# Kernel tuning notes

Measured on AMD Instinct MI355X. Metric: run time of the kernel, lower is better.

## Reference

```python
import jax, jax.numpy as jnp
from jax import lax
import numpy as np

B, T, D, H, OUT = 64, 1024, 256, 512, 256

def _uniform(key, shape, bound):
    return jax.random.uniform(key, shape, jnp.float32, -bound, bound)

def setup_inputs() -> dict:
    key = jax.random.key(0)
    ks = jax.random.split(key, 12)
    bnd = 1.0 / np.sqrt(H)
    inp = {
        "input": jax.random.normal(ks[0], (B, T, D), jnp.float32),
        # layer 0: input_size -> hidden_size
        "W_ih0": _uniform(ks[1], (4 * H, D), bnd),
        "W_hh0": _uniform(ks[2], (4 * H, H), bnd),
        "b_ih0": _uniform(ks[3], (4 * H,), bnd),
        "b_hh0": _uniform(ks[4], (4 * H,), bnd),
        # layer 1: hidden_size -> hidden_size
        "W_ih1": _uniform(ks[5], (4 * H, H), bnd),
        "W_hh1": _uniform(ks[6], (4 * H, H), bnd),
        "b_ih1": _uniform(ks[7], (4 * H,), bnd),
        "b_hh1": _uniform(ks[8], (4 * H,), bnd),
        # final projection
        "fc_w": _uniform(ks[9], (OUT, H), bnd),
        "fc_b": _uniform(ks[10], (OUT,), bnd),
    }
    return inp

def _lstm_layer(x_seq, W_ih, W_hh, b_ih, b_hh):
    # x_seq: [T, B, Din] -> hidden sequence [T, B, H]
    Bb = x_seq.shape[1]
    Hh = W_hh.shape[1]
    # precompute input-to-hidden projection for all timesteps (one big GEMM)
    xW = jnp.einsum("tbd,gd->tbg", x_seq, W_ih) + b_ih + b_hh  # [T, B, 4H]

    def step(carry, xw):
        h, c = carry
        gates = xw + h @ W_hh.T  # [B, 4H]
        i, f, g, o = jnp.split(gates, 4, axis=-1)
        c_new = jax.nn.sigmoid(f) * c + jax.nn.sigmoid(i) * jnp.tanh(g)
        h_new = jax.nn.sigmoid(o) * jnp.tanh(c_new)
        return (h_new, c_new), h_new

    init = (jnp.zeros((Bb, Hh), x_seq.dtype), jnp.zeros((Bb, Hh), x_seq.dtype))
    _, hs = lax.scan(step, init, xW)
    return hs  # [T, B, H]

def reference(input, W_ih0, W_hh0, b_ih0, b_hh0, W_ih1, W_hh1, b_ih1, b_hh1, fc_w, fc_b):
    x = jnp.transpose(input, (1, 0, 2))  # [T, B, D], matches input.permute(1,0,2)
    h1 = _lstm_layer(x, W_ih0, W_hh0, b_ih0, b_hh0)   # layer 0 over all timesteps
    h2 = _lstm_layer(h1, W_ih1, W_hh1, b_ih1, b_hh1)  # layer 1 consumes layer-0 outputs
    last = h2[-1]  # outs[-1].squeeze(): [B, H] (squeeze is a no-op here)
    return last @ fc_w.T + fc_b  # [B, OUT]
```

## Files before the change

### kernel.cpp

```cpp
#include <hip/hip_runtime.h>
#include <hip/hip_bf16.h>
#include <stdint.h>

typedef short short8 __attribute__((ext_vector_type(8)));
typedef float f32x4  __attribute__((ext_vector_type(4)));
typedef float fvec4  __attribute__((ext_vector_type(4)));

#define SCOPE_AGENT __HIP_MEMORY_SCOPE_AGENT
#define MFMA(a,b,c) __builtin_amdgcn_mfma_f32_16x16x32_bf16((a),(b),(c),0,0,0)

constexpr int nT = 1024, nD = 256, nH = 512, nO = 256;
constexpr int SLOT_ELEMS = 64 * 1024;
constexpr size_t SLOT_BYTES = (size_t)SLOT_ELEMS * 2;
constexpr size_t RING_OFF = 8192;
constexpr int NEG = -0x40000000;

#define K4(M)  M(0) M(1) M(2) M(3)
#define GK2(M) M(0,0) M(1,0) M(2,0) M(3,0) M(0,1) M(1,1) M(2,1) M(3,1)
#define GK4(M) GK2(M) M(0,2) M(1,2) M(2,2) M(3,2) M(0,3) M(1,3) M(2,3) M(3,3)

__device__ __forceinline__ float sigm(float x){ return 1.f/(1.f + __expf(-x)); }

__device__ __forceinline__ short8 cvt8h(const float* p){
  fvec4 a = *(const fvec4*)p;
  fvec4 b = *(const fvec4*)(p + 4);
  short8 hi;
  #pragma unroll
  for (int j = 0; j < 8; j++){
    float v = (j < 4) ? a[j] : b[j-4];
    hi[j] = (short)__bfloat16_as_ushort(__float2bfloat16(v));
  }
  return hi;
}

__device__ __forceinline__ void cvt8(const float* p, short8& hi, short8& lo){
  fvec4 a = *(const fvec4*)p;
  fvec4 b = *(const fvec4*)(p + 4);
  #pragma unroll
  for (int j = 0; j < 8; j++){
    float v = (j < 4) ? a[j] : b[j-4];
    __hip_bfloat16 h = __float2bfloat16(v);
    float r = v - __bfloat162float(h);
    hi[j] = (short)__bfloat16_as_ushort(h);
    lo[j] = (short)__bfloat16_as_ushort(__float2bfloat16(r));
  }
}

__device__ __forceinline__ unsigned pack2(float a, float b){
  return (unsigned)__bfloat16_as_ushort(__float2bfloat16(a)) |
         ((unsigned)__bfloat16_as_ushort(__float2bfloat16(b)) << 16);
}
__device__ __forceinline__ unsigned pack2lo(float a, float b){
  float ra = a - __bfloat162float(__float2bfloat16(a));
  float rb = b - __bfloat162float(__float2bfloat16(b));
  return pack2(ra, rb);
}

template<int FAST>
__device__ __forceinline__ short8 ldh(const short* p){
  if constexpr (FAST){
    return *(const short8*)p;
  } else {
    union { unsigned long long u[2]; short8 v; } r;
    const unsigned long long* q = (const unsigned long long*)p;
    r.u[0] = __hip_atomic_load(q,     __ATOMIC_RELAXED, SCOPE_AGENT);
    r.u[1] = __hip_atomic_load(q + 1, __ATOMIC_RELAXED, SCOPE_AGENT);
    return r.v;
  }
}

__device__ __forceinline__ void poll(const int* fb, int t0, int t1){
  if (threadIdx.x < 64){
    int lid = threadIdx.x;
    int tgt = (lid < 32) ? t0 : t1;
    const int* p = fb + lid;
    int spins = 0;
    for(;;){
      int v = __hip_atomic_load(p, __ATOMIC_RELAXED, SCOPE_AGENT);
      if (__all(v >= tgt)) break;
      if (++spins > (1<<17)) break;
      if (spins > 64) __builtin_amdgcn_s_sleep(1);
    }
  }
  __syncthreads();
}

template<int FAST>
__global__ __launch_bounds__(256, 1)
__attribute__((amdgpu_waves_per_eu(1, 1)))
void lstm_kernel(
    const float* __restrict__ x,
    const float* __restrict__ Wih0, const float* __restrict__ Whh0,
    const float* __restrict__ bih0, const float* __restrict__ bhh0,
    const float* __restrict__ Wih1, const float* __restrict__ Whh1,
    const float* __restrict__ bih1, const float* __restrict__ bhh1,
    const float* __restrict__ fcw, const float* __restrict__ fcb,
    float* __restrict__ out,
    short* __restrict__ h1r, short* __restrict__ h2r,
    float* __restrict__ h2last, int* __restrict__ flags, int* __restrict__ arrive)
{
  constexpr int S1M = FAST ? 31 : 7;
  constexpr int S2M = FAST ? 31 : 3;
  constexpr int BPS = FAST ? 24 : 8;

  const int bid   = blockIdx.x;
  const int layer = bid & 1;
  const int bs    = (bid >> 1) & 3;
  const int ns    = bid >> 3;
  const int tid   = threadIdx.x;
  const int w     = tid >> 6;
  const int l     = tid & 63;
  const int lm    = l & 15;
  const int ke    = (l >> 4) << 3;
  const int kw4   = w << 2;
  const int kw2   = w << 1;

  int* fb     = flags + (bs << 6);
  int* myflag = fb + (layer << 5) + ns;

  __shared__ float glds[4][4][16][17];

  __builtin_amdgcn_fence(__ATOMIC_SEQ_CST, "agent");
  __syncthreads();
  if (tid == 0) __hip_atomic_fetch_add(arrive, 1, __ATOMIC_RELAXED, SCOPE_AGENT);
  if (tid < 64){
    int spins = 0;
    while (__hip_atomic_load(arrive, __ATOMIC_RELAXED, SCOPE_AGENT) < 256){
      if (++spins > (1<<20)) break;
      __builtin_amdgcn_s_sleep(1);
    }
  }
  __syncthreads();

  #define GCOL(g) ((g<<9) + (ns<<4) + lm)
  const int brow = (bs << 4) + lm;
  const int bl   = tid >> 4, jj = tid & 15;
  const int hcolbase = ns << 4;

  float c_reg = 0.f;
  float bia0, bia1, bia2, bia3;
  {
    const float* bi = layer ? bih1 : bih0;
    const float* bh = layer ? bhh1 : bhh0;
    int c0 = (ns<<4) + jj;
    bia0 = bi[c0]      + bh[c0];
    bia1 = bi[512+c0]  + bh[512+c0];
    bia2 = bi[1024+c0] + bh[1024+c0];
    bia3 = bi[1536+c0] + bh[1536+c0];
  }

  #define GWR(g) { _Pragma("unroll")                                            \
    for (int r = 0; r < 4; r++) glds[w][g][((l>>4)<<2)+r][lm] = p##g[r]; }
  #define CELLX(SLOTBASE, T, LAST)                                              \
  {                                                                             \
    GWR(0) GWR(1) GWR(2) GWR(3)                                                 \
    __syncthreads();                                                            \
    float gi = glds[0][0][bl][jj]+glds[1][0][bl][jj]+glds[2][0][bl][jj]+glds[3][0][bl][jj]+bia0; \
    float gf = glds[0][1][bl][jj]+glds[1][1][bl][jj]+glds[2][1][bl][jj]+glds[3][1][bl][jj]+bia1; \
    float gg = glds[0][2][bl][jj]+glds[1][2][bl][jj]+glds[2][2][bl][jj]+glds[3][2][bl][jj]+bia2; \
    float go = glds[0][3][bl][jj]+glds[1][3][bl][jj]+glds[2][3][bl][jj]+glds[3][3][bl][jj]+bia3; \
    float cn = sigm(gf)*c_reg + sigm(gi)*tanhf(gg);                             \
    c_reg = cn;                                                                 \
    float hn  = sigm(go)*tanhf(cn);                                             \
    float hn2 = __shfl_down(hn, 1);                                             \
    if (!(jj & 1)){                                                             \
      short* p = (SLOTBASE) + bl*1024 + hcolbase + jj;                          \
      __hip_atomic_store((unsigned*)p,       pack2(hn,hn2),   __ATOMIC_RELAXED, SCOPE_AGENT); \
      __hip_atomic_store((unsigned*)(p+512), pack2lo(hn,hn2), __ATOMIC_RELAXED, SCOPE_AGENT); \
    }                                                                           \
    if (LAST)                                                                   \
      __hip_atomic_store(h2last + (size_t)((bs<<4)+bl)*nH + hcolbase + jj, hn,  \
                         __ATOMIC_RELAXED, SCOPE_AGENT);                        \
    __syncthreads();             \
    if (tid == 0)                                                               \
      __hip_atomic_store(myflag, (T), __ATOMIC_RELAXED, SCOPE_AGENT);           \
  }

  if (layer == 0){
    #define DWX(g,i) short8 wxh##g##_##i;
    GK2(DWX)
    #define LWX(g,i) wxh##g##_##i = cvt8h(Wih0 + (size_t)GCOL(g)*nD + (kw2+i)*32 + ke);
    GK2(LWX)
    #define DWH(g,i) short8 whh##g##_##i;
    GK4(DWH)
    #define LWH(g,i) whh##g##_##i = cvt8h(Whh0 + (size_t)GCOL(g)*nH + (kw4+i)*32 + ke);
    GK4(LWH)

    f32x4 xc0={0,0,0,0}, xc1={0,0,0,0}, xc2={0,0,0,0}, xc3={0,0,0,0};
    {
      const float* xb = x + ((size_t)brow*nT)*nD + ke + kw2*32;
      short8 th0, tl0, th1, tl1;
      cvt8(xb, th0, tl0); cvt8(xb + 32, th1, tl1);
      #define XM0(g,i) xc##g = MFMA(th##i, wxh##g##_##i, xc##g);                \
                       xc##g = MFMA(tl##i, wxh##g##_##i, xc##g);
      GK2(XM0)
    }

    for (int t = 0; t < nT; t++){
      poll(fb, t-1, t-BPS);
      if constexpr (FAST)
        if ((t & 15) == 0) __builtin_amdgcn_fence(__ATOMIC_ACQUIRE, "agent");
      const short* hb = h1r + (size_t)((t+S1M)&S1M)*SLOT_ELEMS + brow*1024;
      #define HLD0(i) short8 vh##i = ldh<FAST>(hb + (kw4+i)*32 + ke);           \
                      short8 vl##i = ldh<FAST>(hb + 512 + (kw4+i)*32 + ke);
      K4(HLD0)
      f32x4 xn0={0,0,0,0}, xn1={0,0,0,0}, xn2={0,0,0,0}, xn3={0,0,0,0};
      if (t + 1 < nT){
        const float* xb = x + ((size_t)brow*nT + (t+1))*nD + ke + kw2*32;
        short8 th0, tl0, th1, tl1;
        cvt8(xb, th0, tl0); cvt8(xb + 32, th1, tl1);
        #define XMN(g,i) xn##g = MFMA(th##i, wxh##g##_##i, xn##g);              \
                         xn##g = MFMA(tl##i, wxh##g##_##i, xn##g);
        GK2(XMN)
      }
      f32x4 p0a=xc0, p1a=xc1, p2a=xc2, p3a=xc3;
      f32x4 p0b={0,0,0,0}, p1b={0,0,0,0}, p2b={0,0,0,0}, p3b={0,0,0,0};
      #define HMM0(g,i) { f32x4& d = (i<2) ? p##g##a : p##g##b;                 \
        d = MFMA(vh##i, whh##g##_##i, d); d = MFMA(vl##i, whh##g##_##i, d); }
      GK4(HMM0)
      f32x4 p0=p0a+p0b, p1=p1a+p1b, p2=p2a+p2b, p3=p3a+p3b;
      CELLX(h1r + (size_t)(t&S1M)*SLOT_ELEMS + (bs<<4)*1024, t, 0)
      xc0 = xn0; xc1 = xn1; xc2 = xn2; xc3 = xn3;
    }
  } else {
    #define DWA(g,i) short8 ahh##g##_##i;
    GK4(DWA)
    #define LWA(g,i) ahh##g##_##i = cvt8h(Whh1 + (size_t)GCOL(g)*nH + (kw4+i)*32 + ke);
    GK4(LWA)
    #define DWB(g,i) short8 bwh##g##_##i;
    GK4(DWB)
    #define LWB(g,i) bwh##g##_##i = cvt8h(Wih1 + (size_t)GCOL(g)*nH + (kw4+i)*32 + ke);
    GK4(LWB)

    for (int t = 0; t < nT; t++){
      poll(fb, t, t-1);
      if constexpr (FAST)
        if ((t & 15) == 0) __builtin_amdgcn_fence(__ATOMIC_ACQUIRE, "agent");
      const short* h2b = h2r + (size_t)((t+S2M)&S2M)*SLOT_ELEMS + brow*1024;
      const short* h1b = h1r + (size_t)(t&S1M)*SLOT_ELEMS + brow*1024;
      #define HLD2(i) short8 u2h##i = ldh<FAST>(h2b + (kw4+i)*32 + ke);         \
                      short8 u2l##i = ldh<FAST>(h2b + 512 + (kw4+i)*32 + ke);
      K4(HLD2)
      #define HLD1(i) short8 u1h##i = ldh<FAST>(h1b + (kw4+i)*32 + ke);         \
                      short8 u1l##i = ldh<FAST>(h1b + 512 + (kw4+i)*32 + ke);
      K4(HLD1)
      f32x4 p0a={0,0,0,0}, p1a={0,0,0,0}, p2a={0,0,0,0}, p3a={0,0,0,0};
      f32x4 p0b={0,0,0,0}, p1b={0,0,0,0}, p2b={0,0,0,0}, p3b={0,0,0,0};
      #define HMM2(g,i) { f32x4& d = (i<2) ? p##g##a : p##g##b;                 \
        d = MFMA(u2h##i, ahh##g##_##i, d); d = MFMA(u2l##i, ahh##g##_##i, d); }
      GK4(HMM2)
      #define HMM1(g,i) { f32x4& d = (i<2) ? p##g##a : p##g##b;                 \
        d = MFMA(u1h##i, bwh##g##_##i, d); d = MFMA(u1l##i, bwh##g##_##i, d); }
      GK4(HMM1)
      f32x4 p0=p0a+p0b, p1=p1a+p1b, p2=p2a+p2b, p3=p3a+p3b;
      CELLX(h2r + (size_t)(t&S2M)*SLOT_ELEMS + (bs<<4)*1024, t, (t == nT-1))
    }

    if (ns < 16){
      poll(fb, NEG, nT-1);
      const int orow = (bs<<4) + bl;
      const int ocol = (ns<<4) + jj;
      const unsigned long long* hq = (const unsigned long long*)(h2last + (size_t)orow*nH);
      const float* wr = fcw + (size_t)ocol*nH;
      float s0=0.f, s1=0.f, s2=0.f, s3=0.f;
      #pragma unroll 8
      for (int k = 0; k < nH; k += 8){
        union{ unsigned long long u; float f[2]; } q0,q1,q2,q3;
        q0.u = __hip_atomic_load(hq + (k>>1)    , __ATOMIC_RELAXED, SCOPE_AGENT);
        q1.u = __hip_atomic_load(hq + (k>>1) + 1, __ATOMIC_RELAXED, SCOPE_AGENT);
        q2.u = __hip_atomic_load(hq + (k>>1) + 2, __ATOMIC_RELAXED, SCOPE_AGENT);
        q3.u = __hip_atomic_load(hq + (k>>1) + 3, __ATOMIC_RELAXED, SCOPE_AGENT);
        fvec4 w0 = *(const fvec4*)(wr + k);
        fvec4 w1 = *(const fvec4*)(wr + k + 4);
        s0 += q0.f[0]*w0[0] + q0.f[1]*w0[1];
        s1 += q1.f[0]*w0[2] + q1.f[1]*w0[3];
        s2 += q2.f[0]*w1[0] + q2.f[1]*w1[1];
        s3 += q3.f[0]*w1[2] + q3.f[1]*w1[3];
      }
      out[(size_t)orow*nO + ocol] = s0 + s1 + s2 + s3 + fcb[ocol];
    }
  }
}

extern "C" void kernel_launch(void* const* d_in, const int* in_sizes, int n_in,
                              void* d_out, int out_size, void* d_ws, size_t ws_size,
                              hipStream_t stream)
{
  char* ws = (char*)d_ws;
  int* flags  = (int*)ws;
  int* arrive = (int*)(ws + 2048);

  size_t need_fast = RING_OFF + 64ull*SLOT_BYTES + (size_t)64*512*4 + 4096;
  const int fast = (ws_size >= need_fast) ? 1 : 0;
  const int s1 = fast ? 32 : 8, s2 = fast ? 32 : 4;

  short* h1r = (short*)(ws + RING_OFF);
  short* h2r = h1r + (size_t)s1 * SLOT_ELEMS;
  float* h2last = (float*)(h2r + (size_t)s2 * SLOT_ELEMS);

  hipMemsetAsync(ws, 0xFF, 1024, stream);
  hipMemsetAsync(ws + 2048, 0, 64, stream);
  hipMemsetAsync(h1r + (size_t)(s1-1)*SLOT_ELEMS, 0, SLOT_BYTES, stream);
  hipMemsetAsync(h2r + (size_t)(s2-1)*SLOT_ELEMS, 0, SLOT_BYTES, stream);

  const float* x    = (const float*)d_in[0];
  const float* Wih0 = (const float*)d_in[1];
  const float* Whh0 = (const float*)d_in[2];
  const float* bih0 = (const float*)d_in[3];
  const float* bhh0 = (const float*)d_in[4];
  const float* Wih1 = (const float*)d_in[5];
  const float* Whh1 = (const float*)d_in[6];
  const float* bih1 = (const float*)d_in[7];
  const float* bhh1 = (const float*)d_in[8];
  const float* fcw  = (const float*)d_in[9];
  const float* fcb  = (const float*)d_in[10];
  float* out = (float*)d_out;

  if (fast)
    lstm_kernel<1><<<256, 256, 0, stream>>>(x, Wih0, Whh0, bih0, bhh0,
        Wih1, Whh1, bih1, bhh1, fcw, fcb, out, h1r, h2r, h2last, flags, arrive);
  else
    lstm_kernel<0><<<256, 256, 0, stream>>>(x, Wih0, Whh0, bih0, bhh0,
        Wih1, Whh1, bih1, bhh1, fcw, fcb, out, h1r, h2r, h2last, flags, arrive);
}
```

Before: 4.546 ms.

## Use per-wave flags, split layer-1 polling, and widen hidden-state stores

Each wave now publishes its own progress flag after waiting on its own stores (vmcnt(0)), which removes the block-wide barrier before signalling. Layer 1 first waits only for layer-0 h1, runs that half of the MFMAs, and only then polls for its own previous h2 step. This overlaps the layer-0 dependency wait with compute. Hidden-state writes are packed into 64-bit atomic stores from every fourth lane. The flag array grows fourfold and pollers now read 128 flags per group, which adds polling traffic. The slow-path BPS also changes from 8 to 7.

```diff
diff --git a/kernel.cpp b/kernel.cpp
--- a/kernel.cpp
+++ b/kernel.cpp
@@ -13,7 +13,6 @@
 constexpr int SLOT_ELEMS = 64 * 1024;
 constexpr size_t SLOT_BYTES = (size_t)SLOT_ELEMS * 2;
 constexpr size_t RING_OFF = 8192;
-constexpr int NEG = -0x40000000;
 
 #define K4(M)  M(0) M(1) M(2) M(3)
 #define GK2(M) M(0,0) M(1,0) M(2,0) M(3,0) M(0,1) M(1,1) M(2,1) M(3,1)
@@ -32,7 +31,6 @@
   }
   return hi;
 }
-
 __device__ __forceinline__ void cvt8(const float* p, short8& hi, short8& lo){
   fvec4 a = *(const fvec4*)p;
   fvec4 b = *(const fvec4*)(p + 4);
@@ -45,7 +43,6 @@
     lo[j] = (short)__bfloat16_as_ushort(__float2bfloat16(r));
   }
 }
-
 __device__ __forceinline__ unsigned pack2(float a, float b){
   return (unsigned)__bfloat16_as_ushort(__float2bfloat16(a)) |
          ((unsigned)__bfloat16_as_ushort(__float2bfloat16(b)) << 16);
@@ -69,15 +66,35 @@
   }
 }
 
-__device__ __forceinline__ void poll(const int* fb, int t0, int t1){
+__device__ __forceinline__ void poll128(const int* b, int tgt){
   if (threadIdx.x < 64){
-    int lid = threadIdx.x;
-    int tgt = (lid < 32) ? t0 : t1;
-    const int* p = fb + lid;
+    const int* p0 = b + threadIdx.x;
+    const int* p1 = b + 64 + threadIdx.x;
     int spins = 0;
     for(;;){
-      int v = __hip_atomic_load(p, __ATOMIC_RELAXED, SCOPE_AGENT);
-      if (__all(v >= tgt)) break;
+      int a = __hip_atomic_load(p0, __ATOMIC_RELAXED, SCOPE_AGENT);
+      int c = __hip_atomic_load(p1, __ATOMIC_RELAXED, SCOPE_AGENT);
+      if (__all((a >= tgt) && (c >= tgt))) break;
+      if (++spins > (1<<17)) break;
+      if (spins > 64) __builtin_amdgcn_s_sleep(1);
+    }
+  }
+  __syncthreads();
+}
+__device__ __forceinline__ void poll_l0(const int* peers, int tp,
+                                        const int* bp, int tb){
+  if (threadIdx.x < 64){
+    const int* p0 = peers + threadIdx.x;
+    const int* p1 = peers + 64 + threadIdx.x;
+    const int* q0 = bp + threadIdx.x;
+    const int* q1 = bp + 64 + threadIdx.x;
+    int spins = 0;
+    for(;;){
+      int a = __hip_atomic_load(p0, __ATOMIC_RELAXED, SCOPE_AGENT);
+      int c = __hip_atomic_load(p1, __ATOMIC_RELAXED, SCOPE_AGENT);
+      int d = __hip_atomic_load(q0, __ATOMIC_RELAXED, SCOPE_AGENT);
+      int e = __hip_atomic_load(q1, __ATOMIC_RELAXED, SCOPE_AGENT);
+      if (__all((a >= tp) && (c >= tp) && (d >= tb) && (e >= tb))) break;
       if (++spins > (1<<17)) break;
       if (spins > 64) __builtin_amdgcn_s_sleep(1);
     }
@@ -101,7 +118,7 @@
 {
   constexpr int S1M = FAST ? 31 : 7;
   constexpr int S2M = FAST ? 31 : 3;
-  constexpr int BPS = FAST ? 24 : 8;
+  constexpr int BPS = FAST ? 24 : 7;
 
   const int bid   = blockIdx.x;
   const int layer = bid & 1;
@@ -115,8 +132,9 @@
   const int kw4   = w << 2;
   const int kw2   = w << 1;
 
-  int* fb     = flags + (bs << 6);
-  int* myflag = fb + (layer << 5) + ns;
+  int* fl0   = flags + (bs << 8);
+  int* fl1   = fl0 + 128;
+  int* myflag = flags + (bs << 8) + (layer << 7) + (ns << 2) + w;
 
   __shared__ float glds[4][4][16][17];
 
@@ -151,8 +169,7 @@
 
   #define GWR(g) { _Pragma("unroll")                                            \
     for (int r = 0; r < 4; r++) glds[w][g][((l>>4)<<2)+r][lm] = p##g[r]; }
-  #define CELLX(SLOTBASE, T, LAST)                                              \
-  {                                                                             \
+  #define CELL_GATES()                                                          \
     GWR(0) GWR(1) GWR(2) GWR(3)                                                 \
     __syncthreads();                                                            \
     float gi = glds[0][0][bl][jj]+glds[1][0][bl][jj]+glds[2][0][bl][jj]+glds[3][0][bl][jj]+bia0; \
@@ -161,19 +178,25 @@
     float go = glds[0][3][bl][jj]+glds[1][3][bl][jj]+glds[2][3][bl][jj]+glds[3][3][bl][jj]+bia3; \
     float cn = sigm(gf)*c_reg + sigm(gi)*tanhf(gg);                             \
     c_reg = cn;                                                                 \
-    float hn  = sigm(go)*tanhf(cn);                                             \
-    float hn2 = __shfl_down(hn, 1);                                             \
-    if (!(jj & 1)){                                                             \
+    float hn = sigm(go)*tanhf(cn);
+
+  #define STORE_H(SLOTBASE, T, LASTST)                                          \
+  {                                                                             \
+    float hn1 = __shfl_down(hn, 1);                                             \
+    unsigned u0  = pack2(hn, hn1),  ul0 = pack2lo(hn, hn1);                     \
+    unsigned u1  = __shfl_down(u0, 2), ul1 = __shfl_down(ul0, 2);               \
+    if (!(jj & 3)){                                                             \
       short* p = (SLOTBASE) + bl*1024 + hcolbase + jj;                          \
-      __hip_atomic_store((unsigned*)p,       pack2(hn,hn2),   __ATOMIC_RELAXED, SCOPE_AGENT); \
-      __hip_atomic_store((unsigned*)(p+512), pack2lo(hn,hn2), __ATOMIC_RELAXED, SCOPE_AGENT); \
+      __hip_atomic_store((unsigned long long*)p,                                \
+          (unsigned long long)u0 | ((unsigned long long)u1 << 32),              \
+          __ATOMIC_RELAXED, SCOPE_AGENT);                                       \
+      __hip_atomic_store((unsigned long long*)(p + 512),                        \
+          (unsigned long long)ul0 | ((unsigned long long)ul1 << 32),            \
+          __ATOMIC_RELAXED, SCOPE_AGENT);                                       \
     }                                                                           \
-    if (LAST)                                                                   \
-      __hip_atomic_store(h2last + (size_t)((bs<<4)+bl)*nH + hcolbase + jj, hn,  \
-                         __ATOMIC_RELAXED, SCOPE_AGENT);                        \
-    __syncthreads();             \
-    if (tid == 0)                                                               \
-      __hip_atomic_store(myflag, (T), __ATOMIC_RELAXED, SCOPE_AGENT);           \
+    LASTST                                                                      \
+    asm volatile("s_waitcnt vmcnt(0)" ::: "memory");         \
+    if (l == 0) __hip_atomic_store(myflag, (T), __ATOMIC_RELAXED, SCOPE_AGENT); \
   }
 
   if (layer == 0){
@@ -197,7 +220,7 @@
     }
 
     for (int t = 0; t < nT; t++){
-      poll(fb, t-1, t-BPS);
+      poll_l0(fl0, t-1, fl1, t-BPS);
       if constexpr (FAST)
         if ((t & 15) == 0) __builtin_amdgcn_fence(__ATOMIC_ACQUIRE, "agent");
       const short* hb = h1r + (size_t)((t+S1M)&S1M)*SLOT_ELEMS + brow*1024;
@@ -219,7 +242,8 @@
         d = MFMA(vh##i, whh##g##_##i, d); d = MFMA(vl##i, whh##g##_##i, d); }
       GK4(HMM0)
       f32x4 p0=p0a+p0b, p1=p1a+p1b, p2=p2a+p2b, p3=p3a+p3b;
-      CELLX(h1r + (size_t)(t&S1M)*SLOT_ELEMS + (bs<<4)*1024, t, 0)
+      CELL_GATES()
+      STORE_H(h1r + (size_t)(t&S1M)*SLOT_ELEMS + (bs<<4)*1024, t, )
       xc0 = xn0; xc1 = xn1; xc2 = xn2; xc3 = xn3;
     }
   } else {
@@ -233,31 +257,36 @@
     GK4(LWB)
 
     for (int t = 0; t < nT; t++){
-      poll(fb, t, t-1);
+      poll128(fl0, t);
       if constexpr (FAST)
         if ((t & 15) == 0) __builtin_amdgcn_fence(__ATOMIC_ACQUIRE, "agent");
-      const short* h2b = h2r + (size_t)((t+S2M)&S2M)*SLOT_ELEMS + brow*1024;
       const short* h1b = h1r + (size_t)(t&S1M)*SLOT_ELEMS + brow*1024;
-      #define HLD2(i) short8 u2h##i = ldh<FAST>(h2b + (kw4+i)*32 + ke);         \
-                      short8 u2l##i = ldh<FAST>(h2b + 512 + (kw4+i)*32 + ke);
-      K4(HLD2)
       #define HLD1(i) short8 u1h##i = ldh<FAST>(h1b + (kw4+i)*32 + ke);         \
                       short8 u1l##i = ldh<FAST>(h1b + 512 + (kw4+i)*32 + ke);
       K4(HLD1)
       f32x4 p0a={0,0,0,0}, p1a={0,0,0,0}, p2a={0,0,0,0}, p3a={0,0,0,0};
       f32x4 p0b={0,0,0,0}, p1b={0,0,0,0}, p2b={0,0,0,0}, p3b={0,0,0,0};
+      #define HMM1(g,i) { f32x4& d = (i<2) ? p##g##a : p##g##b;                 \
+        d = MFMA(u1h##i, bwh##g##_##i, d); d = MFMA(u1l##i, bwh##g##_##i, d); }
+      GK4(HMM1)
+      poll128(fl1, t-1);
+      const short* h2b = h2r + (size_t)((t+S2M)&S2M)*SLOT_ELEMS + brow*1024;
+      #define HLD2(i) short8 u2h##i = ldh<FAST>(h2b + (kw4+i)*32 + ke);         \
+                      short8 u2l##i = ldh<FAST>(h2b + 512 + (kw4+i)*32 + ke);
+      K4(HLD2)
       #define HMM2(g,i) { f32x4& d = (i<2) ? p##g##a : p##g##b;                 \
         d = MFMA(u2h##i, ahh##g##_##i, d); d = MFMA(u2l##i, ahh##g##_##i, d); }
       GK4(HMM2)
-      #define HMM1(g,i) { f32x4& d = (i<2) ? p##g##a : p##g##b;                 \
-        d = MFMA(u1h##i, bwh##g##_##i, d); d = MFMA(u1l##i, bwh##g##_##i, d); }
-      GK4(HMM1)
       f32x4 p0=p0a+p0b, p1=p1a+p1b, p2=p2a+p2b, p3=p3a+p3b;
-      CELLX(h2r + (size_t)(t&S2M)*SLOT_ELEMS + (bs<<4)*1024, t, (t == nT-1))
+      CELL_GATES()
+      STORE_H(h2r + (size_t)(t&S2M)*SLOT_ELEMS + (bs<<4)*1024, t,
+        if (t == nT-1)
+          __hip_atomic_store(h2last + (size_t)((bs<<4)+bl)*nH + hcolbase + jj, hn,
+                             __ATOMIC_RELAXED, SCOPE_AGENT); )
     }
 
     if (ns < 16){
-      poll(fb, NEG, nT-1);
+      poll128(fl1, nT-1);
       const int orow = (bs<<4) + bl;
       const int ocol = (ns<<4) + jj;
       const unsigned long long* hq = (const unsigned long long*)(h2last + (size_t)orow*nH);
@@ -288,7 +317,7 @@
 {
   char* ws = (char*)d_ws;
   int* flags  = (int*)ws;
-  int* arrive = (int*)(ws + 2048);
+  int* arrive = (int*)(ws + 4096);
 
   size_t need_fast = RING_OFF + 64ull*SLOT_BYTES + (size_t)64*512*4 + 4096;
   const int fast = (ws_size >= need_fast) ? 1 : 0;
@@ -298,8 +327,8 @@
   short* h2r = h1r + (size_t)s1 * SLOT_ELEMS;
   float* h2last = (float*)(h2r + (size_t)s2 * SLOT_ELEMS);
 
-  hipMemsetAsync(ws, 0xFF, 1024, stream);
-  hipMemsetAsync(ws + 2048, 0, 64, stream);
+  hipMemsetAsync(ws, 0xFF, 4096, stream);
+  hipMemsetAsync(ws + 4096, 0, 64, stream);
   hipMemsetAsync(h1r + (size_t)(s1-1)*SLOT_ELEMS, 0, SLOT_BYTES, stream);
   hipMemsetAsync(h2r + (size_t)(s2-1)*SLOT_ELEMS, 0, SLOT_BYTES, stream);
 
```

After: 6.276 ms. +38.1%, slower.
